# Kernel optimization log

Hardware: AMD Instinct MI355X
Metric: run time of the kernel (lower is better)

The kernel has to match this reference:

```python
import jax, jax.numpy as jnp
from jax import lax
import numpy as np

NUM_BLOCKS = 50
HIDDEN = 16
KERNEL = 9  # padding = 4 -> 'SAME' for stride 1
B, H, W = 16, 128, 128


def setup_inputs() -> dict:
    key = jax.random.key(0)
    k0, k1, k2, k3, k4 = jax.random.split(key, 5)
    x = jax.random.normal(k0, (B, 1, H, W), jnp.float32)
    # Stacked per-block params; block i uses w1[i, :, :1+i] (rest is padding, never read)
    w1 = jax.random.normal(k1, (NUM_BLOCKS, HIDDEN, 1 + NUM_BLOCKS, KERNEL, KERNEL), jnp.float32) * 0.05
    b1 = jax.random.normal(k2, (NUM_BLOCKS, HIDDEN), jnp.float32) * 0.05
    w2 = jax.random.normal(k3, (NUM_BLOCKS, HIDDEN), jnp.float32) * 0.05  # 1x1 conv to 1 channel
    b2 = jax.random.normal(k4, (NUM_BLOCKS,), jnp.float32) * 0.05
    return {"x": x, "w1": w1, "b1": b1, "w2": w2, "b2": b2}


def reference(x, w1, b1, w2, b2):
    # DenseNet-style growing concat: block i consumes concat of x and all previous outputs.
    feats = x  # [B, 1+i, H, W] at block i
    outs = []
    for i in range(NUM_BLOCKS):
        wi = w1[i, :, : 1 + i]  # [HIDDEN, 1+i, K, K]
        h = lax.conv_general_dilated(
            feats, wi, window_strides=(1, 1), padding="SAME",
            dimension_numbers=("NCHW", "OIHW", "NCHW"))
        h = jax.nn.relu(h + b1[i][None, :, None, None])  # [B, HIDDEN, H, W]
        # 1x1 conv to a single channel + sigmoid
        y = jax.nn.sigmoid(jnp.einsum("bchw,c->bhw", h, w2[i])[:, None] + b2[i])  # [B,1,H,W]
        outs.append(y)
        feats = jnp.concatenate([feats, y], axis=1)
    # Original returns a list of 50 [B,1,H,W] tensors; concatenate along channel dim.
    return jnp.concatenate(outs, axis=1)  # [B, NUM_BLOCKS, H, W]
```

## Files before the change

kernel.cpp:

```cpp
#include <hip/hip_runtime.h>
#include <hip/hip_bf16.h>

#define NBLK 50
#define HID  16
#define BATCH 16
#define HH 128
#define WW 128
#define PH 136
#define PW 136
#define NCH 2
#define PXS 32
#define ROWE (PW*PXS)
#define TAPE 512

typedef __attribute__((ext_vector_type(8))) short short8;
typedef __attribute__((ext_vector_type(4))) float floatx4;

static __device__ __forceinline__ unsigned short f2bf(float f) {
    unsigned int u = __float_as_uint(f);
    unsigned int r = (u + 0x7fffu + ((u >> 16) & 1u)) >> 16;
    return (unsigned short)r;
}

static __device__ __forceinline__ int uswz(int v) { return v ^ ((v >> 3) & 7); }
static __device__ __forceinline__ int swz(int px, int kg) { return uswz(px * 4 + kg); }

#define GLD16(gp, lp) __builtin_amdgcn_global_load_lds( \
    (__attribute__((address_space(1))) void*)(void*)(gp), \
    (__attribute__((address_space(3))) void*)(lp), 16, 0, 0)

static __device__ __forceinline__ void stage_row_u(
    const unsigned short* g, unsigned short* l, int tid,
    int NU, int sh, int um1) {
    #pragma unroll
    for (int t = 0; t < 3; ++t) {
        int j = t * 256 + tid;
        if (j < NU) {
            int v  = uswz(j);
            int pg = ((v >> sh) << 2) + (v & um1);
            GLD16((const char*)g + (size_t)uswz(pg) * 16,
                  (char*)l + (size_t)(t * 256 + (tid & ~63)) * 16);
        }
    }
}

__global__ void prep_w(const float* __restrict__ w1, unsigned short* __restrict__ wbuf) {
    int idx = blockIdx.x * 256 + threadIdx.x;
    const int total = NBLK * NCH * 81 * TAPE;
    if (idx >= total) return;
    int e    = idx & 7;
    int lane = (idx >> 3) & 63;
    int tap  = (idx >> 9) % 81;
    int bc   = idx / (81 * TAPE);
    int ch   = bc & 1, blk = bc >> 1;
    int hc   = lane & 15;
    int c    = ch * 32 + (lane >> 4) * 8 + e;
    float v = 0.f;
    if (c <= blk) v = w1[(((size_t)blk * HID + hc) * (1 + NBLK) + c) * 81 + tap];
    wbuf[idx] = f2bf(v);
}

__global__ void zero_halo(unsigned short* __restrict__ feats) {
    int t = blockIdx.x * 256 + threadIdx.x;
    const int PPX = 2112;
    const int TOT = BATCH * NCH * PPX * 4;
    if (t >= TOT) return;
    int w    = t & 3;
    int rest = t >> 2;
    int p    = rest % PPX;
    int ch   = (rest / PPX) % NCH;
    int b    = rest / (PPX * NCH);
    int row, px;
    if (p < 1088) {
        int r4 = p / 136; px = p % 136;
        row = (r4 < 4) ? r4 : r4 + 128;
    } else {
        int q = p - 1088;
        row = 4 + (q >> 3);
        int c = q & 7;
        px = (c < 4) ? c : c + 128;
    }
    float4* dst = (float4*)((char*)feats +
        ((((size_t)b * PH + row) * NCH + ch) * ROWE) * 2 + (size_t)swz(px, w) * 16);
    *dst = make_float4(0.f, 0.f, 0.f, 0.f);
}

__global__ void init_x(const float* __restrict__ x, unsigned short* __restrict__ feats) {
    int idx = blockIdx.x * 256 + threadIdx.x;
    if (idx >= BATCH * HH * WW) return;
    int xw = idx & (WW - 1);
    int yy = (idx >> 7) & (HH - 1);
    int b  = idx >> 14;
    int pp = xw + 4;
    feats[((((size_t)b * PH + (yy + 4)) * NCH)) * ROWE + (size_t)swz(pp, 0) * 8]
        = f2bf(x[idx]);
}

__global__ __launch_bounds__(256, 2) void block_kern(
    unsigned short* feats, const unsigned short* __restrict__ wbuf,
    const float* __restrict__ b1, const float* __restrict__ w2,
    const float* __restrict__ b2, float* __restrict__ out,
    int blk, int nchunk)
{
    __shared__ __align__(16) unsigned short sB[2][ROWE];

    const int xcd = blockIdx.x & 7;
    const int i   = blockIdx.x >> 3;
    const int b   = 2 * xcd + (i >> 5);
    const int s   = i & 31;

    const int tid  = threadIdx.x;
    const int lane = tid & 63;
    const int wv   = tid >> 6;
    const int n    = lane & 15;
    const int kg   = lane >> 4;
    const int x0   = wv * 32;

    floatx4 acc[4][2];
    #pragma unroll
    for (int o = 0; o < 4; ++o)
        #pragma unroll
        for (int t = 0; t < 2; ++t)
            acc[o][t] = (floatx4){0.f, 0.f, 0.f, 0.f};

    const unsigned short* fb = feats + (size_t)b * PH * NCH * ROWE;

    for (int c = 0; c < nchunk; ++c) {
        const unsigned short* wsrc = wbuf + (size_t)(blk * NCH + c) * 81 * TAPE + lane * 8;

        int Kc = blk + 1 - 32 * c;
        if (Kc > 32) Kc = 32;
        const int kgs = (Kc + 7) >> 3;
        const int sh  = (kgs >= 3) ? 2 : (kgs >> 1);
        const int um1 = (1 << sh) - 1;
        const int NU  = 136 << sh;
        const int bvx = ((x0 + n) << sh) + (kg & um1);

        short8 Areg[4][9];
        stage_row_u(fb + (size_t)((4 * s) * NCH + c) * ROWE, &sB[0][0], tid,
                    NU, sh, um1);
        #pragma unroll
        for (int kx = 0; kx < 9; ++kx)
            Areg[0][kx] = *(const short8*)(wsrc + (size_t)kx * TAPE);
        __syncthreads();

        #pragma unroll
        for (int step = 0; step < 12; ++step) {
            if (step < 11)
                stage_row_u(fb + (size_t)((4 * s + step + 1) * NCH + c) * ROWE,
                            &sB[(step + 1) & 1][0], tid, NU, sh, um1);

            const unsigned short* bb = &sB[step & 1][0];
            #pragma unroll
            for (int kx = 0; kx < 9; ++kx) {
                const int v0 = bvx + (kx << sh);
                const int v1 = bvx + ((16 + kx) << sh);
                short8 B0 = *(const short8*)(bb + (size_t)uswz(v0) * 8);
                short8 B1 = *(const short8*)(bb + (size_t)uswz(v1) * 8);
                #pragma unroll
                for (int o = 0; o < 4; ++o) {
                    if (o <= step && step - o <= 8) {
                        acc[o][0] = __builtin_amdgcn_mfma_f32_16x16x32_bf16(
                            Areg[(step - o) & 3][kx], B0, acc[o][0], 0, 0, 0);
                        acc[o][1] = __builtin_amdgcn_mfma_f32_16x16x32_bf16(
                            Areg[(step - o) & 3][kx], B1, acc[o][1], 0, 0, 0);
                    }
                }
            }

            if (step < 8) {
                #pragma unroll
                for (int kx = 0; kx < 9; ++kx)
                    Areg[(step + 1) & 3][kx] =
                        *(const short8*)(wsrc + (size_t)((step + 1) * 9 + kx) * TAPE);
            }
            __syncthreads();
        }
    }

    float b1v[4], w2v[4];
    #pragma unroll
    for (int r = 0; r < 4; ++r) {
        b1v[r] = b1[blk * HID + kg * 4 + r];
        w2v[r] = w2[blk * HID + kg * 4 + r];
    }
    const float bb2 = b2[blk];
    const int cw = blk + 1, cchunk = cw >> 5, cidx = cw & 31;

    #pragma unroll
    for (int o = 0; o < 4; ++o) {
        const int yrow = 4 * s + o;
        #pragma unroll
        for (int t = 0; t < 2; ++t) {
            float p = 0.f;
            #pragma unroll
            for (int r = 0; r < 4; ++r)
                p += fmaxf(acc[o][t][r] + b1v[r], 0.f) * w2v[r];
            p += __shfl_xor(p, 16, 64);
            p += __shfl_xor(p, 32, 64);
            if (kg == 0) {
                float yv = 1.f / (1.f + __expf(-(p + bb2)));
                int px = x0 + 16 * t + n;
                out[(((size_t)b * NBLK + blk) * HH + yrow) * WW + px] = yv;
                int pp = px + 4;
                feats[(((size_t)b * PH + (yrow + 4)) * NCH + cchunk) * ROWE
                      + (size_t)swz(pp, cidx >> 3) * 8 + (cidx & 7)] = f2bf(yv);
            }
        }
    }
}

extern "C" void kernel_launch(void* const* d_in, const int* in_sizes, int n_in,
                              void* d_out, int out_size, void* d_ws, size_t ws_size,
                              hipStream_t stream) {
    const float* x  = (const float*)d_in[0];
    const float* w1 = (const float*)d_in[1];
    const float* b1 = (const float*)d_in[2];
    const float* w2 = (const float*)d_in[3];
    const float* b2 = (const float*)d_in[4];
    float* out = (float*)d_out;

    unsigned short* feats = (unsigned short*)d_ws;
    size_t feats_bytes = (size_t)BATCH * PH * NCH * ROWE * sizeof(unsigned short);
    unsigned short* wbuf = (unsigned short*)((char*)d_ws + feats_bytes);

    const int htotal = BATCH * NCH * 2112 * 4;
    zero_halo<<<(htotal + 255) / 256, 256, 0, stream>>>(feats);
    init_x<<<(BATCH * HH * WW + 255) / 256, 256, 0, stream>>>(x, feats);
    const int wtotal = NBLK * NCH * 81 * TAPE;
    prep_w<<<(wtotal + 255) / 256, 256, 0, stream>>>(w1, wbuf);

    for (int blk = 0; blk < NBLK; ++blk) {
        int nchunk = (blk + 32) / 32;
        block_kern<<<BATCH * 32, 256, 0, stream>>>(feats, wbuf, b1, w2, b2, out, blk, nchunk);
    }
}
```

Measured before the change: 1.368 ms.

## Pack multiple kx taps into MFMA K dimension for narrow channel chunks

When a channel chunk has few active channels, the weight layout now packs several horizontal kernel taps into the 32-wide MFMA K dimension, so each MFMA covers several kx positions instead of mostly zero-padded channels. The chunk loop is templated on the packing shift, so MFMA count per row drops from 9 to 3 or 5 for narrow chunks, and a zero pad is written past the staged row to cover the extra reads. The cost is more template instantiations, larger code, and a more complex weight remap in prep_w.

```diff
diff --git a/kernel.cpp b/kernel.cpp
--- a/kernel.cpp
+++ b/kernel.cpp
@@ -50,13 +50,24 @@
     if (idx >= total) return;
     int e    = idx & 7;
     int lane = (idx >> 3) & 63;
-    int tap  = (idx >> 9) % 81;
+    int slot = (idx >> 9) % 81;
     int bc   = idx / (81 * TAPE);
     int ch   = bc & 1, blk = bc >> 1;
-    int hc   = lane & 15;
-    int c    = ch * 32 + (lane >> 4) * 8 + e;
+    int hc   = lane & 15, kg = lane >> 4;
+    int Kc = blk + 1 - 32 * ch;
+    if (Kc > 32) Kc = 32;
     float v = 0.f;
-    if (c <= blk) v = w1[(((size_t)blk * HID + hc) * (1 + NBLK) + c) * 81 + tap];
+    if (Kc >= 1) {
+        int kgs = (Kc + 7) >> 3;
+        int sh  = (kgs >= 3) ? 2 : (kgs >> 1);
+        int P   = 4 >> sh;
+        int ky  = slot / 9, q = slot % 9;
+        int kx  = q * P + (kg >> sh);
+        int cl  = (kg & ((1 << sh) - 1)) * 8 + e;
+        int c   = ch * 32 + cl;
+        if (kx <= 8 && c <= blk)
+            v = w1[(((size_t)blk * HID + hc) * (1 + NBLK) + c) * 81 + ky * 9 + kx];
+    }
     wbuf[idx] = f2bf(v);
 }
 
@@ -96,6 +107,66 @@
         = f2bf(x[idx]);
 }
 
+template<int SH>
+static __device__ __forceinline__ void chunk_pass(
+    const unsigned short* __restrict__ base,
+    const unsigned short* __restrict__ wsrc,
+    unsigned short (*sB)[ROWE],
+    floatx4 (&acc)[4][2],
+    int tid, int n, int kg, int x0)
+{
+    constexpr int P   = 4 >> SH;
+    constexpr int PT  = (8 + P) / P;
+    constexpr int um1 = (1 << SH) - 1;
+    constexpr int NU  = 136 << SH;
+    const int bvx = ((x0 + n + (kg >> SH)) << SH) + (kg & um1);
+    const size_t rstride = (size_t)NCH * ROWE;
+
+    if constexpr (SH < 2) {
+        if (tid < 16)
+            *(short8*)(&sB[tid >> 3][(size_t)(NU + (tid & 7)) * 8]) =
+                (short8){0, 0, 0, 0, 0, 0, 0, 0};
+    }
+
+    short8 Areg[4][PT];
+    stage_row_u(base, &sB[0][0], tid, NU, SH, um1);
+    #pragma unroll
+    for (int q = 0; q < PT; ++q)
+        Areg[0][q] = *(const short8*)(wsrc + (size_t)q * TAPE);
+    __syncthreads();
+
+    #pragma unroll
+    for (int step = 0; step < 12; ++step) {
+        if (step < 11)
+            stage_row_u(base + (size_t)(step + 1) * rstride,
+                        &sB[(step + 1) & 1][0], tid, NU, SH, um1);
+
+        const unsigned short* bb = &sB[step & 1][0];
+        #pragma unroll
+        for (int q = 0; q < PT; ++q) {
+            short8 B0 = *(const short8*)(bb + (size_t)uswz(bvx + 4 * q) * 8);
+            short8 B1 = *(const short8*)(bb + (size_t)uswz(bvx + (16 << SH) + 4 * q) * 8);
+            #pragma unroll
+            for (int o = 0; o < 4; ++o) {
+                if (o <= step && step - o <= 8) {
+                    acc[o][0] = __builtin_amdgcn_mfma_f32_16x16x32_bf16(
+                        Areg[(step - o) & 3][q], B0, acc[o][0], 0, 0, 0);
+                    acc[o][1] = __builtin_amdgcn_mfma_f32_16x16x32_bf16(
+                        Areg[(step - o) & 3][q], B1, acc[o][1], 0, 0, 0);
+                }
+            }
+        }
+
+        if (step < 8) {
+            #pragma unroll
+            for (int q = 0; q < PT; ++q)
+                Areg[(step + 1) & 3][q] =
+                    *(const short8*)(wsrc + (size_t)((step + 1) * 9 + q) * TAPE);
+        }
+        __syncthreads();
+    }
+}
+
 __global__ __launch_bounds__(256, 2) void block_kern(
     unsigned short* feats, const unsigned short* __restrict__ wbuf,
     const float* __restrict__ b1, const float* __restrict__ w2,
@@ -127,55 +198,13 @@
 
     for (int c = 0; c < nchunk; ++c) {
         const unsigned short* wsrc = wbuf + (size_t)(blk * NCH + c) * 81 * TAPE + lane * 8;
-
+        const unsigned short* base = fb + (size_t)((4 * s) * NCH + c) * ROWE;
         int Kc = blk + 1 - 32 * c;
         if (Kc > 32) Kc = 32;
         const int kgs = (Kc + 7) >> 3;
-        const int sh  = (kgs >= 3) ? 2 : (kgs >> 1);
-        const int um1 = (1 << sh) - 1;
-        const int NU  = 136 << sh;
-        const int bvx = ((x0 + n) << sh) + (kg & um1);
-
-        short8 Areg[4][9];
-        stage_row_u(fb + (size_t)((4 * s) * NCH + c) * ROWE, &sB[0][0], tid,
-                    NU, sh, um1);
-        #pragma unroll
-        for (int kx = 0; kx < 9; ++kx)
-            Areg[0][kx] = *(const short8*)(wsrc + (size_t)kx * TAPE);
-        __syncthreads();
-
-        #pragma unroll
-        for (int step = 0; step < 12; ++step) {
-            if (step < 11)
-                stage_row_u(fb + (size_t)((4 * s + step + 1) * NCH + c) * ROWE,
-                            &sB[(step + 1) & 1][0], tid, NU, sh, um1);
-
-            const unsigned short* bb = &sB[step & 1][0];
-            #pragma unroll
-            for (int kx = 0; kx < 9; ++kx) {
-                const int v0 = bvx + (kx << sh);
-                const int v1 = bvx + ((16 + kx) << sh);
-                short8 B0 = *(const short8*)(bb + (size_t)uswz(v0) * 8);
-                short8 B1 = *(const short8*)(bb + (size_t)uswz(v1) * 8);
-                #pragma unroll
-                for (int o = 0; o < 4; ++o) {
-                    if (o <= step && step - o <= 8) {
-                        acc[o][0] = __builtin_amdgcn_mfma_f32_16x16x32_bf16(
-                            Areg[(step - o) & 3][kx], B0, acc[o][0], 0, 0, 0);
-                        acc[o][1] = __builtin_amdgcn_mfma_f32_16x16x32_bf16(
-                            Areg[(step - o) & 3][kx], B1, acc[o][1], 0, 0, 0);
-                    }
-                }
-            }
-
-            if (step < 8) {
-                #pragma unroll
-                for (int kx = 0; kx < 9; ++kx)
-                    Areg[(step + 1) & 3][kx] =
-                        *(const short8*)(wsrc + (size_t)((step + 1) * 9 + kx) * TAPE);
-            }
-            __syncthreads();
-        }
+        if (kgs >= 3)      chunk_pass<2>(base, wsrc, sB, acc, tid, n, kg, x0);
+        else if (kgs == 2) chunk_pass<1>(base, wsrc, sB, acc, tid, n, kg, x0);
+        else               chunk_pass<0>(base, wsrc, sB, acc, tid, n, kg, x0);
     }
 
     float b1v[4], w2v[4];
```

Result: faster. 1.170 ms (-14.5%).
